# Performance work log

Hardware: AMD Instinct MI355X
Metric: run time of the kernel (lower is better)

The kernel has to match this reference:

```python
import jax, jax.numpy as jnp
import numpy as np

N, C, T, V = 64, 64, 300, 25
IC = 16   # inter_channels = out_channels // coff_embedding
NS = 3    # num_subset


def _conv1x1(x, w, b):
    # x: (n,c,t,v), w: (o,c) -> (n,o,t,v)
    return jnp.einsum('nctv,oc->notv', x, w) + b[None, :, None, None]


def _conv9x1(x, w, b):
    # kernel (9,1) over (T,V), padding (4,0)
    y = jax.lax.conv_general_dilated(x, w, (1, 1), ((4, 4), (0, 0)),
                                     dimension_numbers=('NCHW', 'OIHW', 'NCHW'))
    return y + b[None, :, None, None]


def _attn(f1, f2):
    # f1,f2: (n,ic,t,v) -> softmax over rows (axis -2) of (n,v,v)
    n, ic, t, v = f1.shape
    a1 = f1.transpose(0, 3, 1, 2).reshape(n, v, ic * t)
    a2 = f2.reshape(n, ic * t, v)
    return jax.nn.softmax(jnp.matmul(a1, a2) / (ic * t), axis=-2)


def setup_inputs() -> dict:
    key = jax.random.key(0)
    ks = jax.random.split(key, 21)
    s = 0.05
    return {
        'x': jax.random.normal(ks[0], (N, C, T, V), jnp.float32),
        'weights': jax.random.uniform(ks[1], (8,), jnp.float32),
        'A': jax.random.uniform(ks[2], (NS, V, V), jnp.float32),
        'a_w': jax.random.normal(ks[3], (NS, IC, C), jnp.float32) * s,
        'a_b': jax.random.normal(ks[4], (NS, IC), jnp.float32) * s,
        'b_w': jax.random.normal(ks[5], (NS, IC, C), jnp.float32) * s,
        'b_b': jax.random.normal(ks[6], (NS, IC), jnp.float32) * s,
        'd_w': jax.random.normal(ks[7], (NS, C, C), jnp.float32) * s,
        'd_b': jax.random.normal(ks[8], (NS, C), jnp.float32) * s,
        't1_w': jax.random.normal(ks[9], (NS, IC, C, 9, 1), jnp.float32) * s,
        't1_b': jax.random.normal(ks[10], (NS, IC), jnp.float32) * s,
        't2_w': jax.random.normal(ks[11], (NS, IC, C, 9, 1), jnp.float32) * s,
        't2_b': jax.random.normal(ks[12], (NS, IC), jnp.float32) * s,
        'st11_w1x1': jax.random.normal(ks[13], (2, IC, C), jnp.float32) * s,
        'st11_w9': jax.random.normal(ks[14], (IC, C, 9, 1), jnp.float32) * s,
        'st11_b': jax.random.normal(ks[15], (NS, IC), jnp.float32) * s,
        'st12_w1x1': jax.random.normal(ks[16], (2, IC, C), jnp.float32) * s,
        'st12_w9': jax.random.normal(ks[17], (IC, C, 9, 1), jnp.float32) * s,
        'st12_b': jax.random.normal(ks[18], (NS, IC), jnp.float32) * s,
        'bn_w': jax.random.uniform(ks[19], (C,), jnp.float32),
        'bn_b': jax.random.normal(ks[20], (C,), jnp.float32) * s,
    }


def reference(x, weights, A, a_w, a_b, b_w, b_b, d_w, d_b, t1_w, t1_b,
              t2_w, t2_b, st11_w1x1, st11_w9, st11_b, st12_w1x1, st12_w9,
              st12_b, bn_w, bn_b):
    n, c, t, v = x.shape
    I = jnp.eye(v, dtype=x.dtype)
    # fixed Chebyshev-like adjacency variants (elementwise powers, as in torch.pow)
    A_ch4 = 8 * A**4 - 8 * A**2 + I
    A_ch4s = jax.nn.softmax(A_ch4 / v, axis=-2)
    A_ch3 = 4 * A**3 - 3 * A
    A_ch2 = 2 * A**2 - I
    A_mix = (weights[0] * A + weights[1] * A_ch4s + weights[2] * A_ch4
             + weights[3] * A_ch3 + weights[4] * A_ch2)  # (NS,V,V)

    x_flat = x.reshape(n, c * t, v)
    y = 0.0
    for i in range(NS):
        S_ab = _attn(_conv1x1(x, a_w[i], a_b[i]), _conv1x1(x, b_w[i], b_b[i]))
        S_t = _attn(_conv9x1(x, t1_w[i], t1_b[i]), _conv9x1(x, t2_w[i], t2_b[i]))
        # conv_ST11/12 lists interleave 1x1 and (9,1) convs; index [i] hits: 1x1, (9,1), 1x1
        if i == 1:
            f11 = _conv9x1(x, st11_w9, st11_b[i])
            f12 = _conv9x1(x, st12_w9, st12_b[i])
        else:
            j = 0 if i == 0 else 1
            f11 = _conv1x1(x, st11_w1x1[j], st11_b[i])
            f12 = _conv1x1(x, st12_w1x1[j], st12_b[i])
        S_st = _attn(f11, f12)
        Ai = A_mix[i] + weights[5] * S_ab + weights[6] * S_t + weights[7] * S_st
        z = jnp.matmul(x_flat, Ai).reshape(n, c, t, v)
        y = y + _conv1x1(z, d_w[i], d_b[i])

    # BatchNorm2d in training mode: batch stats over (N,T,V)
    mu = y.mean(axis=(0, 2, 3), keepdims=True)
    var = y.var(axis=(0, 2, 3), keepdims=True)
    yn = (y - mu) / jnp.sqrt(var + 1e-5) * bn_w[None, :, None, None] + bn_b[None, :, None, None]
    # in_channels == out_channels -> down is identity
    return jax.nn.relu(yn + x)
```

## Files before the change

### kernel.cpp

```cpp
#include <hip/hip_runtime.h>

#define N_    64
#define C_    64
#define T_    300
#define V_    25
#define IC_   16
#define TV_   7500
#define CTV_  480000
#define NB_   6400

typedef __attribute__((ext_vector_type(8))) short short8;
typedef __attribute__((ext_vector_type(4))) float f32x4;

static __device__ inline short f2bf(float f) {
    unsigned u = __float_as_uint(f);
    unsigned r = (u + 0x7fff + ((u >> 16) & 1)) >> 16;
    return (short)r;
}
static __device__ inline float bf2f(short s) {
    return __uint_as_float(((unsigned)(unsigned short)s) << 16);
}

__global__ void amix_kernel(const float* __restrict__ A, const float* __restrict__ w,
                            float* __restrict__ amix) {
    int tid = threadIdx.x;
    if (tid >= 75) return;
    int s = tid / 25, col = tid % 25;
    const float* As = A + s * 625;
    float av[25], ch4[25];
#pragma unroll
    for (int r = 0; r < 25; ++r) {
        float a = As[r * 25 + col];
        float a2 = a * a;
        float eye = (r == col) ? 1.f : 0.f;
        av[r] = a;
        ch4[r] = 8.f * a2 * a2 - 8.f * a2 + eye;
    }
    float m = -1e30f;
#pragma unroll
    for (int r = 0; r < 25; ++r) m = fmaxf(m, ch4[r] * (1.f / 25.f));
    float e[25];
    float sum = 0.f;
#pragma unroll
    for (int r = 0; r < 25; ++r) { e[r] = __expf(ch4[r] * (1.f / 25.f) - m); sum += e[r]; }
    float inv = 1.f / sum;
    float w0 = w[0], w1 = w[1], w2 = w[2], w3 = w[3], w4 = w[4];
#pragma unroll
    for (int r = 0; r < 25; ++r) {
        float a = av[r], a2 = a * a;
        float eye = (r == col) ? 1.f : 0.f;
        amix[s * 625 + r * 25 + col] =
            w0 * a + w1 * (e[r] * inv) + w2 * ch4[r] +
            w3 * (4.f * a2 * a - 3.f * a) + w4 * (2.f * a2 - eye);
    }
}

__global__ void wprep_all(
    const float* __restrict__ a_w, const float* __restrict__ b_w,
    const float* __restrict__ t1_w, const float* __restrict__ t2_w,
    const float* __restrict__ st11_w1, const float* __restrict__ st12_w1,
    const float* __restrict__ st11_w9, const float* __restrict__ st12_w9,
    const float* __restrict__ a_b, const float* __restrict__ b_b,
    const float* __restrict__ t1_b, const float* __restrict__ t2_b,
    const float* __restrict__ st11_b, const float* __restrict__ st12_b,
    short* __restrict__ wpk_all, float* __restrict__ bpk) {
    int idx = blockIdx.x * 256 + threadIdx.x;
    int pair, r;
    bool bias_path = false;
    if (idx < 9 * 18432) {
        pair = idx / 18432; r = idx - pair * 18432;
    } else if (idx < 9 * 18432 + 288) {
        bias_path = true;
        int bidx = idx - 9 * 18432;
        pair = bidx >> 5; r = bidx & 31;
    } else return;

    const float *w1, *w2, *bb1, *bb2; int taps;
    switch (pair) {
        case 0: taps=1; w1=a_w;          w2=b_w;          bb1=a_b;       bb2=b_b;       break;
        case 1: taps=9; w1=t1_w;         w2=t2_w;         bb1=t1_b;      bb2=t2_b;      break;
        case 2: taps=1; w1=st11_w1;      w2=st12_w1;      bb1=st11_b;    bb2=st12_b;    break;
        case 3: taps=1; w1=a_w+1024;     w2=b_w+1024;     bb1=a_b+16;    bb2=b_b+16;    break;
        case 4: taps=9; w1=t1_w+9216;    w2=t2_w+9216;    bb1=t1_b+16;   bb2=t2_b+16;   break;
        case 5: taps=9; w1=st11_w9;      w2=st12_w9;      bb1=st11_b+16; bb2=st12_b+16; break;
        case 6: taps=1; w1=a_w+2048;     w2=b_w+2048;     bb1=a_b+32;    bb2=b_b+32;    break;
        case 7: taps=9; w1=t1_w+18432;   w2=t2_w+18432;   bb1=t1_b+32;   bb2=t2_b+32;   break;
        default: taps=1; w1=st11_w1+1024; w2=st12_w1+1024; bb1=st11_b+32; bb2=st12_b+32; break;
    }
    if (bias_path) {
        int half = r >> 4, o = r & 15;
        bpk[pair * 32 + r] = half ? bb2[o] : bb1[o];
        return;
    }
    if (r >= taps * 2048) return;
    int j = r & 7;
    int l = (r >> 3) & 63;
    int half = (r >> 9) & 1;
    int kk = r >> 10;
    int K = kk * 32 + ((l >> 4) << 3) + j;
    int c = K & 63, k = K >> 6;
    int o = l & 15;
    const float* w = half ? w2 : w1;
    wpk_all[pair * 18432 + r] = f2bf(w[(o * 64 + c) * taps + k]);
}

__global__ void dwprep(const float* __restrict__ dw, const float* __restrict__ db,
                       short* __restrict__ dwpk, float* __restrict__ db_sum) {
    int idx = blockIdx.x * 256 + threadIdx.x;
    if (idx < 12288) {
        int j = idx & 7;
        int lane = (idx >> 3) & 63;
        int kk = (idx >> 9) & 1;
        int mt = idx >> 10;
        int R = mt * 16 + (lane & 15);
        int c = kk * 32 + ((lane >> 4) << 3) + j;
        int i = R >> 6, o = R & 63;
        dwpk[idx] = f2bf(dw[i * 4096 + o * 64 + c]);
    }
    if (idx < 64) db_sum[idx] = db[idx] + db[64 + idx] + db[128 + idx];
}

template <int CNT>
static __device__ __attribute__((always_inline)) void conv_onetap(
    const int (&PL)[CNT], const short* __restrict__ wpk_all, const short* xs,
    int pw, int lane, f32x4 (*acc)[2][2]) {
    int q = lane >> 4, m = lane & 15;
#pragma unroll
    for (int kc2 = 0; kc2 < 2; ++kc2) {
        int c0 = kc2 * 32;
        short8 b0 = *(const short8*)(xs + (pw + m + 100) * 72 + c0 + q * 8);
        short8 b1 = *(const short8*)(xs + (pw + m + 116) * 72 + c0 + q * 8);
#pragma unroll
        for (int pi = 0; pi < CNT; ++pi) {
            const short* wp = wpk_all + PL[pi] * 18432 + kc2 * 1024 + lane * 8;
            short8 a0 = *(const short8*)(wp);
            short8 a1 = *(const short8*)(wp + 512);
            acc[pi][0][0] = __builtin_amdgcn_mfma_f32_16x16x32_bf16(a0, b0, acc[pi][0][0], 0, 0, 0);
            acc[pi][0][1] = __builtin_amdgcn_mfma_f32_16x16x32_bf16(a0, b1, acc[pi][0][1], 0, 0, 0);
            acc[pi][1][0] = __builtin_amdgcn_mfma_f32_16x16x32_bf16(a1, b0, acc[pi][1][0], 0, 0, 0);
            acc[pi][1][1] = __builtin_amdgcn_mfma_f32_16x16x32_bf16(a1, b1, acc[pi][1][1], 0, 0, 0);
        }
    }
}

template <int CNT>
static __device__ __attribute__((always_inline)) void conv_ninetap(
    const int (&PL)[CNT], const short* __restrict__ wpk_all, const short* xs,
    int pw, int lane, f32x4 (*acc)[2][2]) {
    int q = lane >> 4, m = lane & 15;
#pragma unroll
    for (int kc = 0; kc < 18; ++kc) {
        int k = kc >> 1;
        int c0 = (kc & 1) * 32;
        short8 b0 = *(const short8*)(xs + (pw + m + 25 * k) * 72 + c0 + q * 8);
        short8 b1 = *(const short8*)(xs + (pw + m + 25 * k + 16) * 72 + c0 + q * 8);
#pragma unroll
        for (int pi = 0; pi < CNT; ++pi) {
            const short* wp = wpk_all + PL[pi] * 18432 + kc * 1024 + lane * 8;
            short8 a0 = *(const short8*)(wp);
            short8 a1 = *(const short8*)(wp + 512);
            acc[pi][0][0] = __builtin_amdgcn_mfma_f32_16x16x32_bf16(a0, b0, acc[pi][0][0], 0, 0, 0);
            acc[pi][0][1] = __builtin_amdgcn_mfma_f32_16x16x32_bf16(a0, b1, acc[pi][0][1], 0, 0, 0);
            acc[pi][1][0] = __builtin_amdgcn_mfma_f32_16x16x32_bf16(a1, b0, acc[pi][1][0], 0, 0, 0);
            acc[pi][1][1] = __builtin_amdgcn_mfma_f32_16x16x32_bf16(a1, b1, acc[pi][1][1], 0, 0, 0);
        }
    }
}

static __device__ __attribute__((always_inline)) void fT_write(
    const f32x4 acc[2][2], int pair, short* fb, const float* __restrict__ bpk,
    int wq, int lane) {
    int q = lane >> 4, m = lane & 15;
    int pw = wq * 32;
    f32x4 bh0 = *(const f32x4*)(bpk + pair * 32 + q * 4);
    f32x4 bh1 = *(const f32x4*)(bpk + pair * 32 + 16 + q * 4);
#pragma unroll
    for (int h = 0; h < 2; ++h) {
#pragma unroll
        for (int nt = 0; nt < 2; ++nt) {
            int p = pw + nt * 16 + m;
            if (p < 125) {
                int tl = p / 25, v = p - tl * 25;
#pragma unroll
                for (int r = 0; r < 4; ++r) {
                    float bv = h ? bh1[r] : bh0[r];
                    fb[h * 3328 + v * 104 + tl * 16 + q * 4 + r] = f2bf(acc[h][nt][r] + bv);
                }
            }
        }
    }
}

static __device__ __attribute__((always_inline)) void gram_store(
    const short* fb, int pair, short* __restrict__ Gpart, int n, int ch,
    int wq, int lane) {
    int q = lane >> 4, m = lane & 15;
    int mt = wq >> 1, ntl = wq & 1;
    f32x4 g = (f32x4)(0.f);
#pragma unroll
    for (int s = 0; s < 3; ++s) {
        short8 af = *(const short8*)(fb + (mt * 16 + m) * 104 + s * 32 + q * 8);
        short8 bf = *(const short8*)(fb + 3328 + (ntl * 16 + m) * 104 + s * 32 + q * 8);
        g = __builtin_amdgcn_mfma_f32_16x16x32_bf16(af, bf, g, 0, 0, 0);
    }
    int gvp = ntl * 16 + m;
    if (gvp < 25) {
        short* gdst = Gpart + ((pair * 64 + n) * 60 + ch) * 625 + gvp;
#pragma unroll
        for (int r = 0; r < 4; ++r) {
            int v = mt * 16 + q * 4 + r;
            if (v < 25) gdst[v * 25] = f2bf(g[r]);
        }
    }
}

__global__ __launch_bounds__(512, 4) void convgram(
    const float* __restrict__ x, const short* __restrict__ wpk_all,
    const float* __restrict__ bpk, short* __restrict__ Gpart) {
    __shared__ __align__(16) short xs[328 * 72];
    __shared__ __align__(16) short fTb[2 * 6656];
    int tid = threadIdx.x;
    int n = blockIdx.y, ch = blockIdx.x;
    int p0 = ch * 125;
    const float* xn = x + n * CTV_;

    for (int g = 0; g < 5; ++g) {
        float vb[8]; int ib[8];
#pragma unroll
        for (int u = 0; u < 8; ++u) {
            int jj = tid + (g * 8 + u) * 512;
            int c = jj / 328, rr = jj - c * 328;
            int pp = p0 - 100 + rr;
            vb[u] = (pp >= 0 && pp < TV_) ? xn[c * TV_ + pp] : 0.f;
            ib[u] = rr * 72 + c;
        }
#pragma unroll
        for (int u = 0; u < 8; ++u) xs[ib[u]] = f2bf(vb[u]);
    }
    {
        int jj = tid + 40 * 512;
        int c = jj / 328, rr = jj - c * 328;
        int pp = p0 - 100 + rr;
        xs[rr * 72 + c] = f2bf((pp >= 0 && pp < TV_) ? xn[c * TV_ + pp] : 0.f);
    }
    for (int jj = tid; jj < 6656; jj += 512) ((int*)fTb)[jj] = 0;
    __syncthreads();

    int wave = tid >> 6, lane = tid & 63;
    int wq = wave & 3, grp = wave >> 2;
    int pw = wq * 32;
    short* fb = fTb + grp * 6656;

    {
        f32x4 acc3[3][2][2];
#pragma unroll
        for (int p = 0; p < 3; ++p)
#pragma unroll
            for (int h = 0; h < 2; ++h)
#pragma unroll
                for (int nt = 0; nt < 2; ++nt) acc3[p][h][nt] = (f32x4)(0.f);
        if (grp == 0) {
            const int PL[3] = {0, 2, 3};
            conv_onetap<3>(PL, wpk_all, xs, pw, lane, acc3);
        } else {
            const int PL[2] = {6, 8};
            conv_onetap<2>(PL, wpk_all, xs, pw, lane, acc3);
        }
        const int pl0[3] = {0, 2, 3}, pl1[3] = {6, 8, 0};
        int npair = (grp == 0) ? 3 : 2;
#pragma unroll
        for (int r = 0; r < 3; ++r) {
            bool valid = r < npair;
            int pair = (grp == 0) ? pl0[r] : pl1[r];
            if (valid) fT_write(acc3[r], pair, fb, bpk, wq, lane);
            __syncthreads();
            if (valid) gram_store(fb, pair, Gpart, n, ch, wq, lane);
            __syncthreads();
        }
    }

    {
        f32x4 acc2[2][2][2];
#pragma unroll
        for (int p = 0; p < 2; ++p)
#pragma unroll
            for (int h = 0; h < 2; ++h)
#pragma unroll
                for (int nt = 0; nt < 2; ++nt) acc2[p][h][nt] = (f32x4)(0.f);
        if (grp == 0) {
            const int PL[2] = {1, 4};
            conv_ninetap<2>(PL, wpk_all, xs, pw, lane, acc2);
        } else {
            const int PL[2] = {5, 7};
            conv_ninetap<2>(PL, wpk_all, xs, pw, lane, acc2);
        }
        const int plA[2] = {1, 4}, plB[2] = {5, 7};
#pragma unroll
        for (int r = 0; r < 2; ++r) {
            int pair = (grp == 0) ? plA[r] : plB[r];
            fT_write(acc2[r], pair, fb, bpk, wq, lane);
            __syncthreads();
            gram_store(fb, pair, Gpart, n, ch, wq, lane);
            __syncthreads();
        }
    }
}

__global__ __launch_bounds__(256) void gram_finalize_all(
    const short* __restrict__ Gpart, float* __restrict__ S) {
    __shared__ float sm[625];
    int n = blockIdx.x, pair = blockIdx.y;
    int tid = threadIdx.x;
    const short* g = Gpart + (pair * 64 + n) * 60 * 625;
    for (int qq = tid; qq < 625; qq += 256) {
        float s = 0.f;
#pragma unroll
        for (int ch = 0; ch < 60; ++ch) s += bf2f(g[ch * 625 + qq]);
        sm[qq] = s * (1.f / 4800.f);
    }
    __syncthreads();
    if (tid < 25) {
        int col = tid;
        float m = -1e30f;
#pragma unroll
        for (int r = 0; r < 25; ++r) m = fmaxf(m, sm[r * 25 + col]);
        float e[25];
        float sum = 0.f;
#pragma unroll
        for (int r = 0; r < 25; ++r) { e[r] = __expf(sm[r * 25 + col] - m); sum += e[r]; }
        float inv = 1.f / sum;
#pragma unroll
        for (int r = 0; r < 25; ++r)
            S[pair * 40000 + n * 625 + r * 25 + col] = e[r] * inv;
    }
}

__global__ __launch_bounds__(256) void aprep(
    const float* __restrict__ amix, const float* __restrict__ S,
    const float* __restrict__ wts, short* __restrict__ apk) {
    int n = blockIdx.x;
    int tid = threadIdx.x;
    float w5 = wts[5], w6 = wts[6], w7 = wts[7];
#pragma unroll
    for (int it = 0; it < 15; ++it) {
        int jj = tid + it * 256;
        int i = jj / 1280;
        int rem = jj - i * 1280;
        int v = rem / 40, vp = rem - v * 40;
        float val = 0.f;
        if (v < 25 && vp < 25) {
            int e = vp * 25 + v;
            val = amix[i * 625 + e]
                + w5 * S[(i * 3 + 0) * 40000 + n * 625 + e]
                + w6 * S[(i * 3 + 1) * 40000 + n * 625 + e]
                + w7 * S[(i * 3 + 2) * 40000 + n * 625 + e];
        }
        apk[n * 3840 + jj] = f2bf(val);
    }
}

__global__ __launch_bounds__(256, 3) void mega(
    const float* __restrict__ x, const short* __restrict__ apk,
    const short* __restrict__ dwpk, const float* __restrict__ db_sum,
    float* __restrict__ out, float* __restrict__ partials) {
    __shared__ __align__(16) short xs[80 * 72];
    __shared__ __align__(16) short us[3 * 64 * 104];

    int tid = threadIdx.x;
    int n = blockIdx.y;
    int t0 = blockIdx.x * 3;
    const float* xn = x + n * CTV_ + t0 * 25;

    int wave = tid >> 6, lane = tid & 63;
    int q = lane >> 4, m = lane & 15;

    short8 af[3][2];
#pragma unroll
    for (int mt = 0; mt < 3; ++mt)
#pragma unroll
        for (int kk = 0; kk < 2; ++kk)
            af[mt][kk] = *(const short8*)(dwpk + ((wave * 3 + mt) * 2 + kk) * 512 + lane * 8);
    const short* an = apk + n * 3840;
    short8 bfr[3][2];
#pragma unroll
    for (int i = 0; i < 3; ++i)
#pragma unroll
        for (int nt = 0; nt < 2; ++nt)
            bfr[i][nt] = *(const short8*)(an + (i * 32 + nt * 16 + m) * 40 + q * 8);
    float db4[4];
#pragma unroll
    for (int r = 0; r < 4; ++r) db4[r] = db_sum[wave * 16 + q * 4 + r];

    {
        float vb[10]; int ib[10];
        for (int g = 0; g < 2; ++g) {
#pragma unroll
            for (int u = 0; u < 10; ++u) {
                int jj = tid + (g * 10 + u) * 256;
                int c = jj / 80, p = jj - c * 80;
                vb[u] = (p < 75) ? xn[c * TV_ + p] : 0.f;
                ib[u] = p * 72 + c;
            }
#pragma unroll
            for (int u = 0; u < 10; ++u) xs[ib[u]] = f2bf(vb[u]);
        }
    }
    for (int jj = tid; jj < 3 * 64 * 52; jj += 256) ((int*)us)[jj] = 0;

    __syncthreads();

    f32x4 acc[3][5];
#pragma unroll
    for (int mt = 0; mt < 3; ++mt)
#pragma unroll
        for (int nt = 0; nt < 5; ++nt) acc[mt][nt] = (f32x4)(0.f);

#pragma unroll
    for (int nt = 0; nt < 5; ++nt) {
        short8 b0 = *(const short8*)(xs + (nt * 16 + m) * 72 + q * 8);
        short8 b1 = *(const short8*)(xs + (nt * 16 + m) * 72 + 32 + q * 8);
#pragma unroll
        for (int mt = 0; mt < 3; ++mt) {
            acc[mt][nt] = __builtin_amdgcn_mfma_f32_16x16x32_bf16(af[mt][0], b0, acc[mt][nt], 0, 0, 0);
            acc[mt][nt] = __builtin_amdgcn_mfma_f32_16x16x32_bf16(af[mt][1], b1, acc[mt][nt], 0, 0, 0);
        }
    }
#pragma unroll
    for (int nt = 0; nt < 5; ++nt) {
        int p = nt * 16 + m;
        if (p < 75) {
            int t = p / 25, vp = p - t * 25;
            int base = t * 6656 + vp;
#pragma unroll
            for (int mt = 0; mt < 3; ++mt) {
#pragma unroll
                for (int r = 0; r < 4; ++r) {
                    int R = wave * 48 + mt * 16 + q * 4 + r;
                    int i = R >> 6, o = R & 63;
                    us[base + o * 104 + i * 32] = f2bf(acc[mt][nt][r]);
                }
            }
        }
    }
    __syncthreads();

    float sr[4] = {0.f, 0.f, 0.f, 0.f}, s2r[4] = {0.f, 0.f, 0.f, 0.f};
    float* yb = out + n * CTV_ + t0 * 25;
#pragma unroll
    for (int t = 0; t < 3; ++t) {
        f32x4 a2[2];
        a2[0] = (f32x4)(0.f);
        a2[1] = (f32x4)(0.f);
#pragma unroll
        for (int i = 0; i < 3; ++i) {
            short8 ua = *(const short8*)(us + t * 6656 + (wave * 16 + m) * 104 + i * 32 + q * 8);
            a2[0] = __builtin_amdgcn_mfma_f32_16x16x32_bf16(ua, bfr[i][0], a2[0], 0, 0, 0);
            a2[1] = __builtin_amdgcn_mfma_f32_16x16x32_bf16(ua, bfr[i][1], a2[1], 0, 0, 0);
        }
#pragma unroll
        for (int nt = 0; nt < 2; ++nt) {
            int v = nt * 16 + m;
            if (v < 25) {
#pragma unroll
                for (int r = 0; r < 4; ++r) {
                    int o = wave * 16 + q * 4 + r;
                    float val = a2[nt][r] + db4[r];
                    yb[o * TV_ + t * 25 + v] = val;
                    sr[r] += val;
                    s2r[r] += val * val;
                }
            }
        }
    }

    int bid = blockIdx.y * 100 + blockIdx.x;
#pragma unroll
    for (int r = 0; r < 4; ++r) {
        float s = sr[r], s2 = s2r[r];
#pragma unroll
        for (int d = 1; d < 16; d <<= 1) {
            s += __shfl_xor(s, d, 64);
            s2 += __shfl_xor(s2, d, 64);
        }
        if (m == 0) {
            int o = wave * 16 + q * 4 + r;
            partials[o * NB_ + bid] = s;
            partials[(64 + o) * NB_ + bid] = s2;
        }
    }
}

__global__ __launch_bounds__(256) void bn_stats(const float* __restrict__ partials,
                                                float* __restrict__ stats) {
    int j = blockIdx.x;
    int tid = threadIdx.x;
    float s = 0.f;
    for (int idx = tid; idx < NB_; idx += 256) s += partials[j * NB_ + idx];
    for (int d = 32; d > 0; d >>= 1) s += __shfl_down(s, d, 64);
    __shared__ float ls[4];
    if ((tid & 63) == 0) ls[tid >> 6] = s;
    __syncthreads();
    if (tid == 0) stats[j] = ls[0] + ls[1] + ls[2] + ls[3];
}

__global__ __launch_bounds__(256) void bn_final4(
    const float* __restrict__ x, const float* __restrict__ stats,
    const float* __restrict__ bnw, const float* __restrict__ bnb,
    float* __restrict__ y) {
    int idx = blockIdx.x * 256 + threadIdx.x;
    int o = (idx / 1875) & 63;
    const float cnt = (float)(N_ * TV_);
    float mu = stats[o] / cnt;
    float var = stats[64 + o] / cnt - mu * mu;
    float inv = rsqrtf(var + 1e-5f);
    float w = bnw[o], b = bnb[o];
    f32x4 yv = ((const f32x4*)y)[idx];
    f32x4 xv = ((const f32x4*)x)[idx];
    f32x4 r;
#pragma unroll
    for (int k = 0; k < 4; ++k) r[k] = fmaxf((yv[k] - mu) * inv * w + b + xv[k], 0.f);
    ((f32x4*)y)[idx] = r;
}

extern "C" void kernel_launch(void* const* d_in, const int* in_sizes, int n_in,
                              void* d_out, int out_size, void* d_ws, size_t ws_size,
                              hipStream_t stream) {
    (void)in_sizes; (void)n_in; (void)out_size; (void)ws_size;
    const float* x     = (const float*)d_in[0];
    const float* wts   = (const float*)d_in[1];
    const float* A     = (const float*)d_in[2];
    const float* a_w   = (const float*)d_in[3];
    const float* a_b   = (const float*)d_in[4];
    const float* b_w   = (const float*)d_in[5];
    const float* b_b   = (const float*)d_in[6];
    const float* d_wp  = (const float*)d_in[7];
    const float* d_bp  = (const float*)d_in[8];
    const float* t1_w  = (const float*)d_in[9];
    const float* t1_b  = (const float*)d_in[10];
    const float* t2_w  = (const float*)d_in[11];
    const float* t2_b  = (const float*)d_in[12];
    const float* st11_w1 = (const float*)d_in[13];
    const float* st11_w9 = (const float*)d_in[14];
    const float* st11_b  = (const float*)d_in[15];
    const float* st12_w1 = (const float*)d_in[16];
    const float* st12_w9 = (const float*)d_in[17];
    const float* st12_b  = (const float*)d_in[18];
    const float* bn_w  = (const float*)d_in[19];
    const float* bn_b  = (const float*)d_in[20];
    float* out = (float*)d_out;

    char* ws = (char*)d_ws;
    float* amix     = (float*)(ws);
    float* stats    = (float*)(ws + 8192);
    float* db_sum   = (float*)(ws + 12288);
    float* S        = (float*)(ws + 16384);
    short* dwpk     = (short*)(ws + 1460224);
    float* bpk      = (float*)(ws + 1486848);
    short* wpk_all  = (short*)(ws + 1490944);
    short* Gpart    = (short*)(ws + 2097152);
    float* partials = (float*)(ws + 46137344);
    short* apk      = (short*)(ws + 49414144);

    amix_kernel<<<1, 128, 0, stream>>>(A, wts, amix);
    dwprep<<<48, 256, 0, stream>>>(d_wp, d_bp, dwpk, db_sum);
    wprep_all<<<650, 256, 0, stream>>>(a_w, b_w, t1_w, t2_w, st11_w1, st12_w1,
                                       st11_w9, st12_w9, a_b, b_b, t1_b, t2_b,
                                       st11_b, st12_b, wpk_all, bpk);
    convgram<<<dim3(60, 64), 512, 0, stream>>>(x, wpk_all, bpk, Gpart);
    gram_finalize_all<<<dim3(64, 9), 256, 0, stream>>>(Gpart, S);
    aprep<<<64, 256, 0, stream>>>(amix, S, wts, apk);
    mega<<<dim3(100, 64), 256, 0, stream>>>(x, apk, dwpk, db_sum, out, partials);
    bn_stats<<<128, 256, 0, stream>>>(partials, stats);
    bn_final4<<<30000, 256, 0, stream>>>(x, stats, bn_w, bn_b, out);
}
```

Measured before the change: 536.7 us.

## Merge prep kernels, fuse finalize with aprep, pre-transpose x to bf16, atomic BN stats

Several changes land together. The three weight and A-mix prep kernels become one launch, and gram finalize is fused with aprep so S never round-trips through global memory. The mega kernel now reads a bf16 channel-last copy of x made by a new transpose kernel instead of converting x in shared memory, and it raises occupancy hints. BN partial sums go out through atomics into memset stats, which removes the bn_stats kernel. It also vectorizes the fT stores, but it adds an extra pass over x and reuses the Gpart buffer for xbf.

```diff
diff --git a/kernel.cpp b/kernel.cpp
--- a/kernel.cpp
+++ b/kernel.cpp
@@ -7,9 +7,9 @@
 #define IC_   16
 #define TV_   7500
 #define CTV_  480000
-#define NB_   6400
 
 typedef __attribute__((ext_vector_type(8))) short short8;
+typedef __attribute__((ext_vector_type(4))) short sh4;
 typedef __attribute__((ext_vector_type(4))) float f32x4;
 
 static __device__ inline short f2bf(float f) {
@@ -21,41 +21,7 @@
     return __uint_as_float(((unsigned)(unsigned short)s) << 16);
 }
 
-__global__ void amix_kernel(const float* __restrict__ A, const float* __restrict__ w,
-                            float* __restrict__ amix) {
-    int tid = threadIdx.x;
-    if (tid >= 75) return;
-    int s = tid / 25, col = tid % 25;
-    const float* As = A + s * 625;
-    float av[25], ch4[25];
-#pragma unroll
-    for (int r = 0; r < 25; ++r) {
-        float a = As[r * 25 + col];
-        float a2 = a * a;
-        float eye = (r == col) ? 1.f : 0.f;
-        av[r] = a;
-        ch4[r] = 8.f * a2 * a2 - 8.f * a2 + eye;
-    }
-    float m = -1e30f;
-#pragma unroll
-    for (int r = 0; r < 25; ++r) m = fmaxf(m, ch4[r] * (1.f / 25.f));
-    float e[25];
-    float sum = 0.f;
-#pragma unroll
-    for (int r = 0; r < 25; ++r) { e[r] = __expf(ch4[r] * (1.f / 25.f) - m); sum += e[r]; }
-    float inv = 1.f / sum;
-    float w0 = w[0], w1 = w[1], w2 = w[2], w3 = w[3], w4 = w[4];
-#pragma unroll
-    for (int r = 0; r < 25; ++r) {
-        float a = av[r], a2 = a * a;
-        float eye = (r == col) ? 1.f : 0.f;
-        amix[s * 625 + r * 25 + col] =
-            w0 * a + w1 * (e[r] * inv) + w2 * ch4[r] +
-            w3 * (4.f * a2 * a - 3.f * a) + w4 * (2.f * a2 - eye);
-    }
-}
-
-__global__ void wprep_all(
+__global__ void prep_all(
     const float* __restrict__ a_w, const float* __restrict__ b_w,
     const float* __restrict__ t1_w, const float* __restrict__ t2_w,
     const float* __restrict__ st11_w1, const float* __restrict__ st12_w1,
@@ -63,61 +29,99 @@
     const float* __restrict__ a_b, const float* __restrict__ b_b,
     const float* __restrict__ t1_b, const float* __restrict__ t2_b,
     const float* __restrict__ st11_b, const float* __restrict__ st12_b,
-    short* __restrict__ wpk_all, float* __restrict__ bpk) {
-    int idx = blockIdx.x * 256 + threadIdx.x;
-    int pair, r;
-    bool bias_path = false;
-    if (idx < 9 * 18432) {
-        pair = idx / 18432; r = idx - pair * 18432;
-    } else if (idx < 9 * 18432 + 288) {
-        bias_path = true;
-        int bidx = idx - 9 * 18432;
-        pair = bidx >> 5; r = bidx & 31;
-    } else return;
-
-    const float *w1, *w2, *bb1, *bb2; int taps;
-    switch (pair) {
-        case 0: taps=1; w1=a_w;          w2=b_w;          bb1=a_b;       bb2=b_b;       break;
-        case 1: taps=9; w1=t1_w;         w2=t2_w;         bb1=t1_b;      bb2=t2_b;      break;
-        case 2: taps=1; w1=st11_w1;      w2=st12_w1;      bb1=st11_b;    bb2=st12_b;    break;
-        case 3: taps=1; w1=a_w+1024;     w2=b_w+1024;     bb1=a_b+16;    bb2=b_b+16;    break;
-        case 4: taps=9; w1=t1_w+9216;    w2=t2_w+9216;    bb1=t1_b+16;   bb2=t2_b+16;   break;
-        case 5: taps=9; w1=st11_w9;      w2=st12_w9;      bb1=st11_b+16; bb2=st12_b+16; break;
-        case 6: taps=1; w1=a_w+2048;     w2=b_w+2048;     bb1=a_b+32;    bb2=b_b+32;    break;
-        case 7: taps=9; w1=t1_w+18432;   w2=t2_w+18432;   bb1=t1_b+32;   bb2=t2_b+32;   break;
-        default: taps=1; w1=st11_w1+1024; w2=st12_w1+1024; bb1=st11_b+32; bb2=st12_b+32; break;
-    }
-    if (bias_path) {
-        int half = r >> 4, o = r & 15;
-        bpk[pair * 32 + r] = half ? bb2[o] : bb1[o];
+    const float* __restrict__ dw, const float* __restrict__ db,
+    const float* __restrict__ A, const float* __restrict__ wts,
+    short* __restrict__ wpk_all, float* __restrict__ bpk,
+    short* __restrict__ dwpk, float* __restrict__ db_sum,
+    float* __restrict__ amix) {
+    int bx = blockIdx.x;
+    int tid = threadIdx.x;
+
+    if (bx < 650) {
+        int idx = bx * 256 + tid;
+        int pair, r;
+        bool bias_path = false;
+        if (idx < 9 * 18432) {
+            pair = idx / 18432; r = idx - pair * 18432;
+        } else if (idx < 9 * 18432 + 288) {
+            bias_path = true;
+            int bidx = idx - 9 * 18432;
+            pair = bidx >> 5; r = bidx & 31;
+        } else return;
+
+        const float *w1, *w2, *bb1, *bb2; int taps;
+        switch (pair) {
+            case 0: taps=1; w1=a_w;          w2=b_w;          bb1=a_b;       bb2=b_b;       break;
+            case 1: taps=9; w1=t1_w;         w2=t2_w;         bb1=t1_b;      bb2=t2_b;      break;
+            case 2: taps=1; w1=st11_w1;      w2=st12_w1;      bb1=st11_b;    bb2=st12_b;    break;
+            case 3: taps=1; w1=a_w+1024;     w2=b_w+1024;     bb1=a_b+16;    bb2=b_b+16;    break;
+            case 4: taps=9; w1=t1_w+9216;    w2=t2_w+9216;    bb1=t1_b+16;   bb2=t2_b+16;   break;
+            case 5: taps=9; w1=st11_w9;      w2=st12_w9;      bb1=st11_b+16; bb2=st12_b+16; break;
+            case 6: taps=1; w1=a_w+2048;     w2=b_w+2048;     bb1=a_b+32;    bb2=b_b+32;    break;
+            case 7: taps=9; w1=t1_w+18432;   w2=t2_w+18432;   bb1=t1_b+32;   bb2=t2_b+32;   break;
+            default: taps=1; w1=st11_w1+1024; w2=st12_w1+1024; bb1=st11_b+32; bb2=st12_b+32; break;
+        }
+        if (bias_path) {
+            int half = r >> 4, o = r & 15;
+            bpk[pair * 32 + r] = half ? bb2[o] : bb1[o];
+            return;
+        }
+        if (r >= taps * 2048) return;
+        int j = r & 7;
+        int l = (r >> 3) & 63;
+        int half = (r >> 9) & 1;
+        int kk = r >> 10;
+        int K = kk * 32 + ((l >> 4) << 3) + j;
+        int c = K & 63, k = K >> 6;
+        int o = l & 15;
+        const float* w = half ? w2 : w1;
+        wpk_all[pair * 18432 + r] = f2bf(w[(o * 64 + c) * taps + k]);
         return;
     }
-    if (r >= taps * 2048) return;
-    int j = r & 7;
-    int l = (r >> 3) & 63;
-    int half = (r >> 9) & 1;
-    int kk = r >> 10;
-    int K = kk * 32 + ((l >> 4) << 3) + j;
-    int c = K & 63, k = K >> 6;
-    int o = l & 15;
-    const float* w = half ? w2 : w1;
-    wpk_all[pair * 18432 + r] = f2bf(w[(o * 64 + c) * taps + k]);
-}
-
-__global__ void dwprep(const float* __restrict__ dw, const float* __restrict__ db,
-                       short* __restrict__ dwpk, float* __restrict__ db_sum) {
-    int idx = blockIdx.x * 256 + threadIdx.x;
-    if (idx < 12288) {
-        int j = idx & 7;
-        int lane = (idx >> 3) & 63;
-        int kk = (idx >> 9) & 1;
-        int mt = idx >> 10;
-        int R = mt * 16 + (lane & 15);
-        int c = kk * 32 + ((lane >> 4) << 3) + j;
-        int i = R >> 6, o = R & 63;
-        dwpk[idx] = f2bf(dw[i * 4096 + o * 64 + c]);
-    }
-    if (idx < 64) db_sum[idx] = db[idx] + db[64 + idx] + db[128 + idx];
+    if (bx < 698) {
+        int idx = (bx - 650) * 256 + tid;
+        if (idx < 12288) {
+            int j = idx & 7;
+            int lane = (idx >> 3) & 63;
+            int kk = (idx >> 9) & 1;
+            int mt = idx >> 10;
+            int R = mt * 16 + (lane & 15);
+            int c = kk * 32 + ((lane >> 4) << 3) + j;
+            int i = R >> 6, o = R & 63;
+            dwpk[idx] = f2bf(dw[i * 4096 + o * 64 + c]);
+        }
+        if (idx < 64) db_sum[idx] = db[idx] + db[64 + idx] + db[128 + idx];
+        return;
+    }
+    if (tid >= 75) return;
+    int s = tid / 25, col = tid % 25;
+    const float* As = A + s * 625;
+    float av[25], ch4[25];
+#pragma unroll
+    for (int r = 0; r < 25; ++r) {
+        float a = As[r * 25 + col];
+        float a2 = a * a;
+        float eye = (r == col) ? 1.f : 0.f;
+        av[r] = a;
+        ch4[r] = 8.f * a2 * a2 - 8.f * a2 + eye;
+    }
+    float m = -1e30f;
+#pragma unroll
+    for (int r = 0; r < 25; ++r) m = fmaxf(m, ch4[r] * (1.f / 25.f));
+    float e[25];
+    float sum = 0.f;
+#pragma unroll
+    for (int r = 0; r < 25; ++r) { e[r] = __expf(ch4[r] * (1.f / 25.f) - m); sum += e[r]; }
+    float inv = 1.f / sum;
+    float w0 = wts[0], w1 = wts[1], w2 = wts[2], w3 = wts[3], w4 = wts[4];
+#pragma unroll
+    for (int r = 0; r < 25; ++r) {
+        float a = av[r], a2 = a * a;
+        float eye = (r == col) ? 1.f : 0.f;
+        amix[s * 625 + r * 25 + col] =
+            w0 * a + w1 * (e[r] * inv) + w2 * ch4[r] +
+            w3 * (4.f * a2 * a - 3.f * a) + w4 * (2.f * a2 - eye);
+    }
 }
 
 template <int CNT>
@@ -181,11 +185,13 @@
             int p = pw + nt * 16 + m;
             if (p < 125) {
                 int tl = p / 25, v = p - tl * 25;
+                sh4 pk;
 #pragma unroll
                 for (int r = 0; r < 4; ++r) {
                     float bv = h ? bh1[r] : bh0[r];
-                    fb[h * 3328 + v * 104 + tl * 16 + q * 4 + r] = f2bf(acc[h][nt][r] + bv);
+                    pk[r] = f2bf(acc[h][nt][r] + bv);
                 }
+                *(sh4*)(fb + h * 3328 + v * 104 + tl * 16 + q * 4) = pk;
             }
         }
     }
@@ -306,70 +312,98 @@
     }
 }
 
-__global__ __launch_bounds__(256) void gram_finalize_all(
-    const short* __restrict__ Gpart, float* __restrict__ S) {
-    __shared__ float sm[625];
-    int n = blockIdx.x, pair = blockIdx.y;
+__global__ __launch_bounds__(256) void finalize_aprep(
+    const short* __restrict__ Gpart, const float* __restrict__ amix,
+    const float* __restrict__ wts, short* __restrict__ apk) {
+    __shared__ float sm[3 * 625];
+    int n = blockIdx.x, i = blockIdx.y;
     int tid = threadIdx.x;
-    const short* g = Gpart + (pair * 64 + n) * 60 * 625;
-    for (int qq = tid; qq < 625; qq += 256) {
-        float s = 0.f;
-#pragma unroll
-        for (int ch = 0; ch < 60; ++ch) s += bf2f(g[ch * 625 + qq]);
-        sm[qq] = s * (1.f / 4800.f);
+#pragma unroll
+    for (int pi = 0; pi < 3; ++pi) {
+        int pair = i * 3 + pi;
+        const short* g = Gpart + (pair * 64 + n) * 60 * 625;
+        for (int qq = tid; qq < 625; qq += 256) {
+            float s = 0.f;
+#pragma unroll
+            for (int ch = 0; ch < 60; ++ch) s += bf2f(g[ch * 625 + qq]);
+            sm[pi * 625 + qq] = s * (1.f / 4800.f);
+        }
     }
     __syncthreads();
-    if (tid < 25) {
-        int col = tid;
+    if (tid < 75) {
+        int pi = tid / 25, col = tid % 25;
+        float* smp = sm + pi * 625;
         float m = -1e30f;
 #pragma unroll
-        for (int r = 0; r < 25; ++r) m = fmaxf(m, sm[r * 25 + col]);
+        for (int r = 0; r < 25; ++r) m = fmaxf(m, smp[r * 25 + col]);
         float e[25];
         float sum = 0.f;
 #pragma unroll
-        for (int r = 0; r < 25; ++r) { e[r] = __expf(sm[r * 25 + col] - m); sum += e[r]; }
+        for (int r = 0; r < 25; ++r) { e[r] = __expf(smp[r * 25 + col] - m); sum += e[r]; }
         float inv = 1.f / sum;
 #pragma unroll
-        for (int r = 0; r < 25; ++r)
-            S[pair * 40000 + n * 625 + r * 25 + col] = e[r] * inv;
-    }
-}
-
-__global__ __launch_bounds__(256) void aprep(
-    const float* __restrict__ amix, const float* __restrict__ S,
-    const float* __restrict__ wts, short* __restrict__ apk) {
-    int n = blockIdx.x;
-    int tid = threadIdx.x;
+        for (int r = 0; r < 25; ++r) smp[r * 25 + col] = e[r] * inv;
+    }
+    __syncthreads();
     float w5 = wts[5], w6 = wts[6], w7 = wts[7];
 #pragma unroll
-    for (int it = 0; it < 15; ++it) {
-        int jj = tid + it * 256;
-        int i = jj / 1280;
-        int rem = jj - i * 1280;
+    for (int it = 0; it < 5; ++it) {
+        int rem = tid + it * 256;
         int v = rem / 40, vp = rem - v * 40;
         float val = 0.f;
         if (v < 25 && vp < 25) {
             int e = vp * 25 + v;
-            val = amix[i * 625 + e]
-                + w5 * S[(i * 3 + 0) * 40000 + n * 625 + e]
-                + w6 * S[(i * 3 + 1) * 40000 + n * 625 + e]
-                + w7 * S[(i * 3 + 2) * 40000 + n * 625 + e];
-        }
-        apk[n * 3840 + jj] = f2bf(val);
-    }
-}
-
-__global__ __launch_bounds__(256, 3) void mega(
-    const float* __restrict__ x, const short* __restrict__ apk,
+            val = amix[i * 625 + e] + w5 * sm[e] + w6 * sm[625 + e] + w7 * sm[1250 + e];
+        }
+        apk[n * 3840 + i * 1280 + rem] = f2bf(val);
+    }
+}
+
+__global__ __launch_bounds__(256) void xbf_prep(
+    const float* __restrict__ x, short* __restrict__ xbf) {
+    __shared__ __align__(16) float tile[64 * 128];
+    int n = blockIdx.y;
+    int p0 = blockIdx.x * 128;
+    int tid = threadIdx.x;
+    const float* xn = x + n * CTV_;
+#pragma unroll
+    for (int it = 0; it < 8; ++it) {
+        int unit = tid + it * 256;
+        int c = unit >> 5, pf = unit & 31;
+        int p = p0 + pf * 4;
+        f32x4 v;
+        if (p + 3 < TV_) {
+            v = *(const f32x4*)(xn + c * TV_ + p);
+        } else {
+#pragma unroll
+            for (int j = 0; j < 4; ++j) v[j] = (p + j < TV_) ? xn[c * TV_ + p + j] : 0.f;
+        }
+        *(f32x4*)(tile + c * 128 + pf * 4) = v;
+    }
+    __syncthreads();
+#pragma unroll
+    for (int it = 0; it < 4; ++it) {
+        int unit = tid + it * 256;
+        int pp = unit >> 3, cb = unit & 7;
+        if (p0 + pp < TV_) {
+            short8 o;
+#pragma unroll
+            for (int k = 0; k < 8; ++k) o[k] = f2bf(tile[(cb * 8 + k) * 128 + pp]);
+            *(short8*)(xbf + ((size_t)n * TV_ + p0 + pp) * 64 + cb * 8) = o;
+        }
+    }
+}
+
+__global__ __launch_bounds__(256, 4) void mega(
+    const short* __restrict__ xbf, const short* __restrict__ apk,
     const short* __restrict__ dwpk, const float* __restrict__ db_sum,
-    float* __restrict__ out, float* __restrict__ partials) {
-    __shared__ __align__(16) short xs[80 * 72];
+    float* __restrict__ out, float* __restrict__ stats) {
     __shared__ __align__(16) short us[3 * 64 * 104];
 
     int tid = threadIdx.x;
     int n = blockIdx.y;
     int t0 = blockIdx.x * 3;
-    const float* xn = x + n * CTV_ + t0 * 25;
+    const short* xb = xbf + (size_t)n * TV_ * 64 + t0 * 25 * 64;
 
     int wave = tid >> 6, lane = tid & 63;
     int q = lane >> 4, m = lane & 15;
@@ -391,23 +425,7 @@
 #pragma unroll
     for (int r = 0; r < 4; ++r) db4[r] = db_sum[wave * 16 + q * 4 + r];
 
-    {
-        float vb[10]; int ib[10];
-        for (int g = 0; g < 2; ++g) {
-#pragma unroll
-            for (int u = 0; u < 10; ++u) {
-                int jj = tid + (g * 10 + u) * 256;
-                int c = jj / 80, p = jj - c * 80;
-                vb[u] = (p < 75) ? xn[c * TV_ + p] : 0.f;
-                ib[u] = p * 72 + c;
-            }
-#pragma unroll
-            for (int u = 0; u < 10; ++u) xs[ib[u]] = f2bf(vb[u]);
-        }
-    }
-    for (int jj = tid; jj < 3 * 64 * 52; jj += 256) ((int*)us)[jj] = 0;
-
-    __syncthreads();
+    for (int jj = tid; jj < 2496; jj += 256) *(short8*)(us + jj * 8) = (short8)(short)0;
 
     f32x4 acc[3][5];
 #pragma unroll
@@ -417,14 +435,18 @@
 
 #pragma unroll
     for (int nt = 0; nt < 5; ++nt) {
-        short8 b0 = *(const short8*)(xs + (nt * 16 + m) * 72 + q * 8);
-        short8 b1 = *(const short8*)(xs + (nt * 16 + m) * 72 + 32 + q * 8);
+        int pl = nt * 16 + m;
+        bool ok = pl < 75;
+        const short* bp = xb + pl * 64 + q * 8;
+        short8 b0 = ok ? *(const short8*)(bp) : (short8)(short)0;
+        short8 b1 = ok ? *(const short8*)(bp + 32) : (short8)(short)0;
 #pragma unroll
         for (int mt = 0; mt < 3; ++mt) {
             acc[mt][nt] = __builtin_amdgcn_mfma_f32_16x16x32_bf16(af[mt][0], b0, acc[mt][nt], 0, 0, 0);
             acc[mt][nt] = __builtin_amdgcn_mfma_f32_16x16x32_bf16(af[mt][1], b1, acc[mt][nt], 0, 0, 0);
         }
     }
+    __syncthreads();
 #pragma unroll
     for (int nt = 0; nt < 5; ++nt) {
         int p = nt * 16 + m;
@@ -473,7 +495,6 @@
         }
     }
 
-    int bid = blockIdx.y * 100 + blockIdx.x;
 #pragma unroll
     for (int r = 0; r < 4; ++r) {
         float s = sr[r], s2 = s2r[r];
@@ -484,23 +505,10 @@
         }
         if (m == 0) {
             int o = wave * 16 + q * 4 + r;
-            partials[o * NB_ + bid] = s;
-            partials[(64 + o) * NB_ + bid] = s2;
-        }
-    }
-}
-
-__global__ __launch_bounds__(256) void bn_stats(const float* __restrict__ partials,
-                                                float* __restrict__ stats) {
-    int j = blockIdx.x;
-    int tid = threadIdx.x;
-    float s = 0.f;
-    for (int idx = tid; idx < NB_; idx += 256) s += partials[j * NB_ + idx];
-    for (int d = 32; d > 0; d >>= 1) s += __shfl_down(s, d, 64);
-    __shared__ float ls[4];
-    if ((tid & 63) == 0) ls[tid >> 6] = s;
-    __syncthreads();
-    if (tid == 0) stats[j] = ls[0] + ls[1] + ls[2] + ls[3];
+            atomicAdd(&stats[o], s);
+            atomicAdd(&stats[64 + o], s2);
+        }
+    }
 }
 
 __global__ __launch_bounds__(256) void bn_final4(
@@ -551,25 +559,23 @@
 
     char* ws = (char*)d_ws;
     float* amix     = (float*)(ws);
-    float* stats    = (float*)(ws + 8192);
-    float* db_sum   = (float*)(ws + 12288);
-    float* S        = (float*)(ws + 16384);
-    short* dwpk     = (short*)(ws + 1460224);
-    float* bpk      = (float*)(ws + 1486848);
-    short* wpk_all  = (short*)(ws + 1490944);
-    short* Gpart    = (short*)(ws + 2097152);
-    float* partials = (float*)(ws + 46137344);
-    short* apk      = (short*)(ws + 49414144);
-
-    amix_kernel<<<1, 128, 0, stream>>>(A, wts, amix);
-    dwprep<<<48, 256, 0, stream>>>(d_wp, d_bp, dwpk, db_sum);
-    wprep_all<<<650, 256, 0, stream>>>(a_w, b_w, t1_w, t2_w, st11_w1, st12_w1,
-                                       st11_w9, st12_w9, a_b, b_b, t1_b, t2_b,
-                                       st11_b, st12_b, wpk_all, bpk);
+    float* stats    = (float*)(ws + 32768);
+    float* db_sum   = (float*)(ws + 36864);
+    float* bpk      = (float*)(ws + 40960);
+    short* dwpk     = (short*)(ws + 49152);
+    short* wpk_all  = (short*)(ws + 81920);
+    short* apk      = (short*)(ws + 425984);
+    short* Gpart    = (short*)(ws + 1048576);
+    short* xbf      = (short*)(ws + 1048576);
+
+    prep_all<<<699, 256, 0, stream>>>(a_w, b_w, t1_w, t2_w, st11_w1, st12_w1,
+                                      st11_w9, st12_w9, a_b, b_b, t1_b, t2_b,
+                                      st11_b, st12_b, d_wp, d_bp, A, wts,
+                                      wpk_all, bpk, dwpk, db_sum, amix);
+    hipMemsetAsync(stats, 0, 512, stream);
     convgram<<<dim3(60, 64), 512, 0, stream>>>(x, wpk_all, bpk, Gpart);
-    gram_finalize_all<<<dim3(64, 9), 256, 0, stream>>>(Gpart, S);
-    aprep<<<64, 256, 0, stream>>>(amix, S, wts, apk);
-    mega<<<dim3(100, 64), 256, 0, stream>>>(x, apk, dwpk, db_sum, out, partials);
-    bn_stats<<<128, 256, 0, stream>>>(partials, stats);
+    finalize_aprep<<<dim3(64, 3), 256, 0, stream>>>(Gpart, amix, wts, apk);
+    xbf_prep<<<dim3(59, 64), 256, 0, stream>>>(x, xbf);
+    mega<<<dim3(100, 64), 256, 0, stream>>>(xbf, apk, dwpk, db_sum, out, stats);
     bn_final4<<<30000, 256, 0, stream>>>(x, stats, bn_w, bn_b, out);
 }
```

After: 1.114 ms. 108% more time.
